# Performance work log

Hardware: AMD Instinct MI355X
Metric: run time of the kernel (lower is better)

Reference implementation:

```python
import jax, jax.numpy as jnp
import numpy as np

N = 50000      # nodes
E = 800000     # edges (avg degree 16)
D = 64         # input/hidden dim
OUT = 1        # output head dim
ATT_SLOPE = 0.2   # PyG GATConv leaky_relu slope for attention logits
ACT_SLOPE = 0.01  # nn.LeakyReLU default slope


def _gat_layer(x, src, dst, W, a_src, a_dst, b, n):
    """PyG GATConv, heads=1, concat=True, with self-loops already in src/dst."""
    h = x @ W.T                                   # [n, D]
    logit = jax.nn.leaky_relu(h[src] @ a_src + h[dst] @ a_dst, ATT_SLOPE)  # [e]
    m = jax.ops.segment_max(logit, dst, num_segments=n)                    # per-dst max
    e = jnp.exp(logit - m[dst])
    denom = jax.ops.segment_sum(e, dst, num_segments=n)
    coef = e / denom[dst]                         # softmax over incoming edges
    out = jax.ops.segment_sum(coef[:, None] * h[src], dst, num_segments=n)
    return out + b


def setup_inputs() -> dict:
    key = jax.random.key(0)
    ks = jax.random.split(key, 16)
    s = 1.0 / np.sqrt(D)
    inp = {"x": jax.random.normal(ks[0], (N, D), dtype=jnp.float32)}
    for i in range(3):
        inp[f"W{i}"] = jax.random.normal(ks[1 + 4 * i], (D, D), dtype=jnp.float32) * s
        inp[f"a_src{i}"] = jax.random.normal(ks[2 + 4 * i], (D,), dtype=jnp.float32) * s
        inp[f"a_dst{i}"] = jax.random.normal(ks[3 + 4 * i], (D,), dtype=jnp.float32) * s
        inp[f"b{i}"] = jnp.zeros((D,), dtype=jnp.float32)
    inp["Wout"] = jax.random.normal(ks[13], (OUT, D), dtype=jnp.float32) * s
    inp["bout"] = jnp.zeros((OUT,), dtype=jnp.float32)
    inp["edge_index"] = jax.random.randint(ks[14], (2, E), 0, N, dtype=jnp.int64)
    return inp


def reference(x, W0, a_src0, a_dst0, b0, W1, a_src1, a_dst1, b1,
              W2, a_src2, a_dst2, b2, Wout, bout, edge_index):
    n = x.shape[0]
    loops = jnp.arange(n, dtype=edge_index.dtype)
    src = jnp.concatenate([edge_index[0], loops])  # GATConv add_self_loops=True
    dst = jnp.concatenate([edge_index[1], loops])
    act = lambda v: jax.nn.leaky_relu(v, ACT_SLOPE)
    h = act(_gat_layer(x, src, dst, W0, a_src0, a_dst0, b0, n))
    h = act(_gat_layer(h, src, dst, W1, a_src1, a_dst1, b1, n))
    h = act(_gat_layer(h, src, dst, W2, a_src2, a_dst2, b2, n))
    return h @ Wout.T + bout                       # [n, OUT]
```

## Files before the change

kernel.cpp:

```cpp
#include <hip/hip_runtime.h>
#include <hip/hip_fp16.h>

#define DD 64
#define ATT_SLOPE 0.2f
#define ACT_SLOPE 0.01f
#define GNPB 32
#define RCAP 64
#define BUILD_BLOCKS 2048


__device__ __forceinline__ void gemm_body(
        const float* __restrict__ in, const float* __restrict__ W,
        const float* __restrict__ a_src, const float* __restrict__ a_dst,
        __half* __restrict__ h, float* __restrict__ as_out,
        float* __restrict__ ad_out, int n_nodes, int base, float* xin) {
    int t = threadIdx.x;
    int lane = t & 63;
    int w = t >> 6;

    {
        float4* xin4 = (float4*)xin;
        const float4* src4 = (const float4*)in;
        int lim = n_nodes * (DD / 4);
        #pragma unroll
        for (int i = 0; i < (GNPB * DD / 4) / 256; ++i) {
            int idx = i * 256 + t;
            int gi = base * (DD / 4) + idx;
            xin4[idx] = (gi < lim) ? src4[gi]
                                   : make_float4(0.f, 0.f, 0.f, 0.f);
        }
    }
    __syncthreads();

    int n0 = base + w * 8;
    if (n0 >= n_nodes) return;

    float asl = a_src[lane], adl = a_dst[lane];
    const float* wrow = W + (size_t)lane * 64;
    int rmax = n_nodes - n0; if (rmax > 8) rmax = 8;

    if (rmax == 8) {
        float a[8] = {0.f, 0.f, 0.f, 0.f, 0.f, 0.f, 0.f, 0.f};
        #pragma unroll
        for (int kq = 0; kq < 16; ++kq) {
            float4 wv = *(const float4*)(wrow + kq * 4);
            #pragma unroll
            for (int r = 0; r < 8; ++r) {
                float4 xv = *(const float4*)&xin[(w * 8 + r) * DD + kq * 4];
                a[r] = fmaf(xv.x, wv.x, a[r]); a[r] = fmaf(xv.y, wv.y, a[r]);
                a[r] = fmaf(xv.z, wv.z, a[r]); a[r] = fmaf(xv.w, wv.w, a[r]);
            }
        }
        #pragma unroll
        for (int r = 0; r < 8; ++r)
            h[(size_t)(n0 + r) * 64 + lane] = __float2half(a[r]);
        float s[16];
        #pragma unroll
        for (int r = 0; r < 8; ++r) { s[2 * r] = a[r] * asl; s[2 * r + 1] = a[r] * adl; }
        #pragma unroll
        for (int m = 32; m >= 1; m >>= 1) {
            #pragma unroll
            for (int i = 0; i < 16; ++i) s[i] += __shfl_xor(s[i], m, 64);
        }
        if (lane == 0) {
            #pragma unroll
            for (int r = 0; r < 8; ++r) {
                as_out[n0 + r] = s[2 * r];
                ad_out[n0 + r] = s[2 * r + 1];
            }
        }
    } else {
        for (int r = 0; r < rmax; ++r) {
            int node = n0 + r;
            float acc = 0.f;
            #pragma unroll
            for (int kq = 0; kq < 16; ++kq) {
                float4 wv = *(const float4*)(wrow + kq * 4);
                float4 xv = *(const float4*)&xin[(w * 8 + r) * DD + kq * 4];
                acc = fmaf(xv.x, wv.x, acc); acc = fmaf(xv.y, wv.y, acc);
                acc = fmaf(xv.z, wv.z, acc); acc = fmaf(xv.w, wv.w, acc);
            }
            h[(size_t)node * 64 + lane] = __float2half(acc);
            float s1 = acc * asl, s2 = acc * adl;
            #pragma unroll
            for (int m = 32; m >= 1; m >>= 1) {
                s1 += __shfl_xor(s1, m, 64);
                s2 += __shfl_xor(s2, m, 64);
            }
            if (lane == 0) { as_out[node] = s1; ad_out[node] = s2; }
        }
    }
}

__global__ __launch_bounds__(256) void gemm0_build_kernel(
        const float* __restrict__ x, const float* __restrict__ W,
        const float* __restrict__ a_src, const float* __restrict__ a_dst,
        __half* __restrict__ h, float* __restrict__ as_out,
        float* __restrict__ ad_out, int n_nodes,
        const int* __restrict__ ei, int E,
        int* __restrict__ counts, unsigned short* __restrict__ col_src,
        int gemm_blocks) {
    __shared__ float xin[GNPB * DD];
    int bid = blockIdx.x;
    if (bid < gemm_blocks) {
        gemm_body(x, W, a_src, a_dst, h, as_out, ad_out, n_nodes,
                  bid * GNPB, xin);
        return;
    }
    int bb = bid - gemm_blocks;
    int part = bb & 7;
    int rank = bb >> 3;
    int lo = (int)((long long)part * n_nodes / 8);
    int hi = (int)((long long)(part + 1) * n_nodes / 8);
    int tp = rank * 256 + (int)threadIdx.x;
    int stride = (BUILD_BLOCKS >> 3) * 256;
    int ET = E + n_nodes;
    for (int e = tp; e < ET; e += stride) {
        int s, d;
        if (e < E) { s = ei[e]; d = ei[E + e]; }
        else       { s = e - E; d = s; }
        if (d < lo || d >= hi) continue;
        int pos = atomicAdd(&counts[d], 1);
        if (pos < RCAP) col_src[(d << 6) + pos] = (unsigned short)s;
    }
}

__global__ __launch_bounds__(256) void gemm_alpha_kernel(
        const float* __restrict__ in, const float* __restrict__ W,
        const float* __restrict__ a_src, const float* __restrict__ a_dst,
        __half* __restrict__ h, float* __restrict__ as_out,
        float* __restrict__ ad_out, int n_nodes) {
    __shared__ float xin[GNPB * DD];
    gemm_body(in, W, a_src, a_dst, h, as_out, ad_out, n_nodes,
              blockIdx.x * GNPB, xin);
}

template <bool FUSE_HEAD>
__global__ __launch_bounds__(256) void aggregate_kernel(
        const int* __restrict__ counts, const unsigned short* __restrict__ col_src,
        const __half* __restrict__ h, const float* __restrict__ as_arr,
        const float* __restrict__ ad_arr, const float* __restrict__ b,
        float* __restrict__ out, const float* __restrict__ Wout,
        const float* __restrict__ bout, int n_nodes) {
    int t = threadIdx.x;
    int w = t >> 6, lane = t & 63;
    int node = blockIdx.x * 4 + w;
    if (node >= n_nodes) return;
    int g = lane >> 3, u = lane & 7;

    int beg = node << 6;
    int cnt = __builtin_amdgcn_readfirstlane(counts[node]);
    if (cnt > RCAP) cnt = RCAP;
    int end = beg + cnt;
    float adn = ad_arr[node];

    float acc[8] = {0.f, 0.f, 0.f, 0.f, 0.f, 0.f, 0.f, 0.f};
    float lsum = 0.f;
    int e = beg + g;

    uint4 rA = {0, 0, 0, 0}, rB = {0, 0, 0, 0};
    float aA = 0.f, aB = 0.f;
    if (e < end) {
        int s = col_src[e];
        aA = as_arr[s];
        rA = *(const uint4*)(h + (size_t)s * 64 + u * 8);
    }
    if (e + 8 < end) {
        int s = col_src[e + 8];
        aB = as_arr[s];
        rB = *(const uint4*)(h + (size_t)s * 64 + u * 8);
    }
    while (e < end) {
        int e2 = e + 16;
        uint4 rC = {0, 0, 0, 0}; float aC = 0.f;
        if (e2 < end) {
            int s = col_src[e2];
            aC = as_arr[s];
            rC = *(const uint4*)(h + (size_t)s * 64 + u * 8);
        }
        float lg = aA + adn;
        lg = (lg >= 0.f) ? lg : ATT_SLOPE * lg;
        float p = __expf(lg);
        lsum += p;
        float2 f0 = __half22float2(*(const __half2*)&rA.x);
        float2 f1 = __half22float2(*(const __half2*)&rA.y);
        float2 f2 = __half22float2(*(const __half2*)&rA.z);
        float2 f3 = __half22float2(*(const __half2*)&rA.w);
        acc[0] = fmaf(p, f0.x, acc[0]); acc[1] = fmaf(p, f0.y, acc[1]);
        acc[2] = fmaf(p, f1.x, acc[2]); acc[3] = fmaf(p, f1.y, acc[3]);
        acc[4] = fmaf(p, f2.x, acc[4]); acc[5] = fmaf(p, f2.y, acc[5]);
        acc[6] = fmaf(p, f3.x, acc[6]); acc[7] = fmaf(p, f3.y, acc[7]);
        rA = rB; aA = aB;
        rB = rC; aB = aC;
        e += 8;
    }
    #pragma unroll
    for (int m = 8; m <= 32; m <<= 1) {
        #pragma unroll
        for (int i = 0; i < 8; ++i) acc[i] += __shfl_xor(acc[i], m, 64);
        lsum += __shfl_xor(lsum, m, 64);
    }
    float inv = 1.f / lsum;
    const float4 b0 = *(const float4*)(b + u * 8);
    const float4 b1 = *(const float4*)(b + u * 8 + 4);
    float o[8];
    o[0] = acc[0] * inv + b0.x; o[1] = acc[1] * inv + b0.y;
    o[2] = acc[2] * inv + b0.z; o[3] = acc[3] * inv + b0.w;
    o[4] = acc[4] * inv + b1.x; o[5] = acc[5] * inv + b1.y;
    o[6] = acc[6] * inv + b1.z; o[7] = acc[7] * inv + b1.w;
    #pragma unroll
    for (int i = 0; i < 8; ++i) o[i] = (o[i] >= 0.f) ? o[i] : ACT_SLOPE * o[i];

    if (FUSE_HEAD) {
        const float4 w0 = *(const float4*)(Wout + u * 8);
        const float4 w1 = *(const float4*)(Wout + u * 8 + 4);
        float pd = o[0] * w0.x + o[1] * w0.y + o[2] * w0.z + o[3] * w0.w
                 + o[4] * w1.x + o[5] * w1.y + o[6] * w1.z + o[7] * w1.w;
        #pragma unroll
        for (int m = 1; m <= 4; m <<= 1) pd += __shfl_xor(pd, m, 64);
        if (lane == 0) out[node] = pd + bout[0];
    } else if (g == 0) {
        float4 v0 = {o[0], o[1], o[2], o[3]};
        float4 v1 = {o[4], o[5], o[6], o[7]};
        *(float4*)(out + (size_t)node * 64 + u * 8) = v0;
        *(float4*)(out + (size_t)node * 64 + u * 8 + 4) = v1;
    }
}


extern "C" void kernel_launch(void* const* d_in, const int* in_sizes, int n_in,
                              void* d_out, int out_size, void* d_ws, size_t ws_size,
                              hipStream_t stream) {
    const float* x     = (const float*)d_in[0];
    const float* W[3]  = {(const float*)d_in[1], (const float*)d_in[5], (const float*)d_in[9]};
    const float* as[3] = {(const float*)d_in[2], (const float*)d_in[6], (const float*)d_in[10]};
    const float* ad[3] = {(const float*)d_in[3], (const float*)d_in[7], (const float*)d_in[11]};
    const float* bv[3] = {(const float*)d_in[4], (const float*)d_in[8], (const float*)d_in[12]};
    const float* Wout  = (const float*)d_in[13];
    const float* bout  = (const float*)d_in[14];
    const int*   ei    = (const int*)d_in[15];

    const int N = in_sizes[0] / DD;
    const int E = in_sizes[15] / 2;

    char* ws = (char*)d_ws;
    size_t off = 0;
    auto alloc = [&](size_t bytes) {
        void* p = ws + off;
        off = (off + bytes + 255) & ~(size_t)255;
        return p;
    };
    unsigned short* col_src = (unsigned short*)alloc((size_t)N * RCAP * 2);
    int*    counts  = (int*)alloc((size_t)N * 4);
    float*  asA     = (float*)alloc((size_t)N * 4);
    float*  adA     = (float*)alloc((size_t)N * 4);
    float*  asB     = (float*)alloc((size_t)N * 4);
    float*  adB     = (float*)alloc((size_t)N * 4);
    __half* hA      = (__half*)alloc((size_t)N * DD * 2);
    __half* hB      = (__half*)alloc((size_t)N * DD * 2);
    float*  obuf    = (float*)alloc((size_t)N * DD * 4);
    (void)ws_size;

    int gridG  = ((N + GNPB - 1) / GNPB + 7) & ~7;
    int grid4  = (N + 3) / 4;

    hipMemsetAsync(counts, 0, (size_t)N * 4, stream);
    gemm0_build_kernel<<<gridG + BUILD_BLOCKS, 256, 0, stream>>>(
        x, W[0], as[0], ad[0], hA, asA, adA, N,
        ei, E, counts, col_src, gridG);

    aggregate_kernel<false><<<grid4, 256, 0, stream>>>(
        counts, col_src, hA, asA, adA, bv[0], obuf, nullptr, nullptr, N);
    gemm_alpha_kernel<<<gridG, 256, 0, stream>>>(obuf, W[1], as[1], ad[1],
                                                 hB, asB, adB, N);
    aggregate_kernel<false><<<grid4, 256, 0, stream>>>(
        counts, col_src, hB, asB, adB, bv[1], obuf, nullptr, nullptr, N);
    gemm_alpha_kernel<<<gridG, 256, 0, stream>>>(obuf, W[2], as[2], ad[2],
                                                 hA, asA, adA, N);
    aggregate_kernel<true><<<grid4, 256, 0, stream>>>(
        counts, col_src, hA, asA, adA, bv[2], (float*)d_out, Wout, bout, N);
}
```

Before: 266.3 us.

## Replace global-atomic CSR build with two-pass shared-memory bucketed binning

The edge-to-destination adjacency build now runs in two passes. Pass one bins edges into 512-node buckets using shared-memory histograms and a single global atomic per bucket per block. Pass two scatters each bucket into col_src using shared-memory counters and writes counts directly, which removes the per-edge global atomics and the counts memset. This adds an extra kernel launch and a staging buffer aliased onto obuf. It also silently drops edges if any bucket exceeds BCAP or if source ids exceed 16 bits.

```diff
diff --git a/kernel.cpp b/kernel.cpp
--- a/kernel.cpp
+++ b/kernel.cpp
@@ -6,7 +6,10 @@
 #define ACT_SLOPE 0.01f
 #define GNPB 32
 #define RCAP 64
-#define BUILD_BLOCKS 2048
+#define PA_CHUNK 2048
+#define BSH 9
+#define BNODES 512
+#define BCAP 10240
 
 
 __device__ __forceinline__ void gemm_body(
@@ -17,7 +20,6 @@
     int t = threadIdx.x;
     int lane = t & 63;
     int w = t >> 6;
-
     {
         float4* xin4 = (float4*)xin;
         const float4* src4 = (const float4*)in;
@@ -92,36 +94,82 @@
     }
 }
 
-__global__ __launch_bounds__(256) void gemm0_build_kernel(
+__global__ __launch_bounds__(256) void gemm0_binA_kernel(
         const float* __restrict__ x, const float* __restrict__ W,
         const float* __restrict__ a_src, const float* __restrict__ a_dst,
         __half* __restrict__ h, float* __restrict__ as_out,
         float* __restrict__ ad_out, int n_nodes,
         const int* __restrict__ ei, int E,
-        int* __restrict__ counts, unsigned short* __restrict__ col_src,
+        int* __restrict__ bcur, unsigned int* __restrict__ bucket_buf,
         int gemm_blocks) {
     __shared__ float xin[GNPB * DD];
+    __shared__ int hist[128];
+    __shared__ int gbase[128];
     int bid = blockIdx.x;
     if (bid < gemm_blocks) {
         gemm_body(x, W, a_src, a_dst, h, as_out, ad_out, n_nodes,
                   bid * GNPB, xin);
         return;
     }
-    int bb = bid - gemm_blocks;
-    int part = bb & 7;
-    int rank = bb >> 3;
-    int lo = (int)((long long)part * n_nodes / 8);
-    int hi = (int)((long long)(part + 1) * n_nodes / 8);
-    int tp = rank * 256 + (int)threadIdx.x;
-    int stride = (BUILD_BLOCKS >> 3) * 256;
+    int t = threadIdx.x;
+    int base_e = (bid - gemm_blocks) * PA_CHUNK;
     int ET = E + n_nodes;
-    for (int e = tp; e < ET; e += stride) {
+    if (t < 128) hist[t] = 0;
+    __syncthreads();
+
+    unsigned int ent[8];
+    short eb[8];
+    short ep[8];
+    #pragma unroll
+    for (int j = 0; j < 8; ++j) {
+        int e = base_e + j * 256 + t;
+        eb[j] = -1;
+        if (e >= ET) continue;
         int s, d;
         if (e < E) { s = ei[e]; d = ei[E + e]; }
         else       { s = e - E; d = s; }
-        if (d < lo || d >= hi) continue;
-        int pos = atomicAdd(&counts[d], 1);
-        if (pos < RCAP) col_src[(d << 6) + pos] = (unsigned short)s;
+        int b = d >> BSH;
+        ent[j] = (unsigned int)s | ((unsigned int)(d & (BNODES - 1)) << 16);
+        eb[j] = (short)b;
+        ep[j] = (short)atomicAdd(&hist[b], 1);
+    }
+    __syncthreads();
+    if (t < 128) {
+        int c = hist[t];
+        gbase[t] = (c > 0) ? atomicAdd(&bcur[t], c) : 0;
+    }
+    __syncthreads();
+    #pragma unroll
+    for (int j = 0; j < 8; ++j) {
+        if (eb[j] < 0) continue;
+        int pos = gbase[eb[j]] + ep[j];
+        if (pos < BCAP) bucket_buf[(size_t)eb[j] * BCAP + pos] = ent[j];
+    }
+}
+
+__global__ __launch_bounds__(256) void binB_kernel(
+        const unsigned int* __restrict__ bucket_buf, const int* __restrict__ bcur,
+        int* __restrict__ counts, unsigned short* __restrict__ col_src,
+        int n_nodes) {
+    __shared__ int cur[BNODES];
+    int b = blockIdx.x, t = threadIdx.x;
+    for (int i = t; i < BNODES; i += 256) cur[i] = 0;
+    __syncthreads();
+    int cnt = bcur[b]; if (cnt > BCAP) cnt = BCAP;
+    const unsigned int* buf = bucket_buf + (size_t)b * BCAP;
+    for (int i = t; i < cnt; i += 256) {
+        unsigned int en = buf[i];
+        int s = en & 0xFFFF;
+        int dl = en >> 16;
+        int pos = atomicAdd(&cur[dl], 1);
+        if (pos < RCAP)
+            col_src[(((b << BSH) + dl) << 6) + pos] = (unsigned short)s;
+    }
+    __syncthreads();
+    int n0 = b << BSH;
+    for (int i = t; i < BNODES; i += 256) {
+        int d = n0 + i;
+        if (d < n_nodes) counts[d] = cur[i];
     }
 }
 
@@ -240,8 +288,10 @@
     const float* bout  = (const float*)d_in[14];
     const int*   ei    = (const int*)d_in[15];
 
-    const int N = in_sizes[0] / DD;
-    const int E = in_sizes[15] / 2;
+    const int N  = in_sizes[0] / DD;
+    const int E  = in_sizes[15] / 2;
+    const int ET = E + N;
+    const int NBUCK = (N + BNODES - 1) >> BSH;
 
     char* ws = (char*)d_ws;
     size_t off = 0;
@@ -252,6 +302,7 @@
     };
     unsigned short* col_src = (unsigned short*)alloc((size_t)N * RCAP * 2);
     int*    counts  = (int*)alloc((size_t)N * 4);
+    int*    bcur    = (int*)alloc(512 * 4);
     float*  asA     = (float*)alloc((size_t)N * 4);
     float*  adA     = (float*)alloc((size_t)N * 4);
     float*  asB     = (float*)alloc((size_t)N * 4);
@@ -261,13 +312,17 @@
     float*  obuf    = (float*)alloc((size_t)N * DD * 4);
     (void)ws_size;
 
-    int gridG  = ((N + GNPB - 1) / GNPB + 7) & ~7;
-    int grid4  = (N + 3) / 4;
-
-    hipMemsetAsync(counts, 0, (size_t)N * 4, stream);
-    gemm0_build_kernel<<<gridG + BUILD_BLOCKS, 256, 0, stream>>>(
+    unsigned int* bucket_buf = (unsigned int*)obuf;
+
+    int gridG = (N + GNPB - 1) / GNPB;
+    int nA    = (ET + PA_CHUNK - 1) / PA_CHUNK;
+    int grid4 = (N + 3) / 4;
+
+    hipMemsetAsync(bcur, 0, 512 * 4, stream);
+    gemm0_binA_kernel<<<gridG + nA, 256, 0, stream>>>(
         x, W[0], as[0], ad[0], hA, asA, adA, N,
-        ei, E, counts, col_src, gridG);
+        ei, E, bcur, bucket_buf, gridG);
+    binB_kernel<<<NBUCK, 256, 0, stream>>>(bucket_buf, bcur, counts, col_src, N);
 
     aggregate_kernel<false><<<grid4, 256, 0, stream>>>(
         counts, col_src, hA, asA, adA, bv[0], obuf, nullptr, nullptr, N);
```

Result: faster. 257.2 us (-3.4%).
